# Performance work log

Hardware: AMD Instinct MI355X
Metric: run time of the kernel (lower is better)

Reference implementation:

```python
import jax, jax.numpy as jnp
import numpy as np

SHIFTS = (1, 2)          # _GLOBAL_SHIFTS, all < channels so none filtered
LN_EPS = 1e-5


def _layernorm(x, g, b):
    mu = jnp.mean(x, axis=-1, keepdims=True)
    var = jnp.var(x, axis=-1, keepdims=True)
    return (x - mu) * jax.lax.rsqrt(var + LN_EPS) * g + b


def setup_inputs() -> dict:
    key = jax.random.key(0)
    ks = jax.random.split(key, 4)
    B, H, W, D = 8, 96, 96, 256
    n_comp = 2 * len(SHIFTS)  # full mode: dot + wedge per shift
    x = jax.random.normal(ks[0], (B, H, W, D), dtype=jnp.float32)
    # glorot-uniform style scaling for the two dense kernels
    pk = jax.random.normal(ks[1], (n_comp * D, D), dtype=jnp.float32) * (1.0 / np.sqrt(n_comp * D))
    gk = jax.random.normal(ks[2], (2 * D, D), dtype=jnp.float32) * (1.0 / np.sqrt(2 * D))
    return {
        "x": x,
        "ln_gamma": jnp.ones((D,), jnp.float32),
        "ln_beta": jnp.zeros((D,), jnp.float32),
        "proj_kernel": pk,
        "proj_bias": jnp.zeros((D,), jnp.float32),
        "gate_kernel": gk,
        "gate_bias": jnp.zeros((D,), jnp.float32),
        "gamma": jnp.full((D,), 1e-5, jnp.float32),  # LayerScale init
    }


def reference(x, ln_gamma, ln_beta, proj_kernel, proj_bias,
              gate_kernel, gate_bias, gamma):
    # ---- pre-norm ----
    h_norm = _layernorm(x, ln_gamma, ln_beta)                 # [B,H,W,D]
    # ---- context stream (ctx_mode='diff'): deviation from spatial mean ----
    z_det = h_norm
    z_ctx = h_norm - jnp.mean(h_norm, axis=(1, 2), keepdims=True)
    # ---- sparse rolling Clifford product (cli_mode='full') ----
    feats = []
    for s in SHIFTS:
        ctx_s = jnp.roll(z_ctx, -s, axis=-1)   # Z_ctx[(c+s) % D]
        det_s = jnp.roll(z_det, -s, axis=-1)   # Z_det[(c+s) % D]
        dot = jax.nn.silu(z_det * ctx_s)                      # inner part
        wedge = z_det * ctx_s - z_ctx * det_s                 # bivector part
        feats.append(dot)
        feats.append(wedge)
    feats = jnp.concatenate(feats, axis=-1)                   # [B,H,W,4D]
    g_feat = feats @ proj_kernel + proj_bias                  # [B,H,W,D]
    # ---- gated geometric residual ----
    gate_in = jnp.concatenate([h_norm, g_feat], axis=-1)      # [B,H,W,2D]
    alpha = jax.nn.sigmoid(gate_in @ gate_kernel + gate_bias)
    h_mix = (jax.nn.silu(h_norm) + alpha * g_feat) * gamma    # LayerScale
    # drop_path_rate == 0.0 -> identity; caller-side residual add
    return x + h_mix
```

## Files before the change

### kernel.cpp

```cpp
#include <hip/hip_runtime.h>
#include <hip/hip_bf16.h>

typedef unsigned short u16;
typedef unsigned int   u32;
typedef __attribute__((ext_vector_type(2))) float f32x2;
typedef __attribute__((ext_vector_type(4))) float f32x4;
typedef __attribute__((ext_vector_type(4))) u32   u32x4;
typedef __attribute__((ext_vector_type(8))) short bf16x8;

#define HWPIX  9216
#define NPIX   73728
#define LN_EPS 1e-5f
#define MROW   64
#define ASTR   40

template<int N> struct IC { static constexpr int value = N; };

__device__ __forceinline__ u16 f2bf(float f){
  u32 u = __builtin_bit_cast(u32, f);
  u += 0x7fffu + ((u >> 16) & 1u);
  return (u16)(u >> 16);
}
__device__ __forceinline__ u32 pkbf(float lo, float hi){
  u32 d;
  asm("v_cvt_pk_bf16_f32 %0, %1, %2" : "=v"(d) : "v"(lo), "v"(hi));
  return d;
}
__device__ __forceinline__ float bfu2f(u16 h){ return __builtin_bit_cast(float, (u32)h << 16); }
__device__ __forceinline__ float fsigmoid(float v){ return __fdividef(1.f, 1.f + __expf(-v)); }
__device__ __forceinline__ float fsilu(float v){ return __fdividef(v, 1.f + __expf(-v)); }

__device__ __forceinline__ void gld16(const u16* g, u16* l){
  __builtin_amdgcn_global_load_lds((const __attribute__((address_space(1))) void*)g,
                                   (__attribute__((address_space(3))) void*)l,
                                   16, 0, 0);
}

__global__ __launch_bounds__(256) void wconv(const float* __restrict__ pk,
                                             const float* __restrict__ gk,
                                             u16* __restrict__ wsdot,
                                             u16* __restrict__ wsgate)
{
  int gid = blockIdx.x * 256 + threadIdx.x;
  int t = gid >> 10, S = gid & 1023;
  int q = (S >> 2) & 15, pp = S & 3, w8 = (S >> 6) & 7, rb = S >> 9;
  int n  = rb * 128 + w8 * 16 + q;
  int kq = pp ^ ((q >> 1) & 3);
  const float* W; int k0; u16* dst;
  if (t < 8)       { W = pk; k0 =       t      * 32 + kq * 8; dst = wsdot  + (size_t)t * 8192; }
  else if (t < 16) { W = pk; k0 = 512 + (t-8)  * 32 + kq * 8; dst = wsdot  + (size_t)t * 8192; }
  else             { W = gk; k0 =       (t-16) * 32 + kq * 8; dst = wsgate + (size_t)(t-16) * 8192; }
  u32 ow[4];
  #pragma unroll
  for (int e = 0; e < 4; ++e) {
    float f0 = W[(size_t)(k0 + 2*e)     * 256 + n];
    float f1 = W[(size_t)(k0 + 2*e + 1) * 256 + n];
    ow[e] = (u32)f2bf(f0) | ((u32)f2bf(f1) << 16);
  }
  *(u32x4*)(dst + (size_t)S * 8) = (u32x4){ow[0], ow[1], ow[2], ow[3]};
}

__global__ __launch_bounds__(256) void prep(const float* __restrict__ x,
                                            const float* __restrict__ g,
                                            const float* __restrict__ bt,
                                            float* __restrict__ mu_rs,
                                            float* __restrict__ partial)
{
  const int bh = blockIdx.x;
  const int tid = threadIdx.x;
  const int wv = tid >> 6, lane = tid & 63;
  const float* xrow = x + (size_t)bh * 96 * 256;
  __shared__ float red[4][256];

  f32x4 gv = *(const f32x4*)(g  + lane * 4);
  f32x4 bv = *(const f32x4*)(bt + lane * 4);
  f32x4 acc = {0.f, 0.f, 0.f, 0.f};

  for (int w = wv; w < 96; w += 4) {
    f32x4 v = *(const f32x4*)(xrow + w * 256 + lane * 4);
    float s  = v[0] + v[1] + v[2] + v[3];
    float s2 = v[0]*v[0] + v[1]*v[1] + v[2]*v[2] + v[3]*v[3];
    #pragma unroll
    for (int m = 1; m < 64; m <<= 1) { s += __shfl_xor(s, m); s2 += __shfl_xor(s2, m); }
    float mu  = s * (1.f / 256.f);
    float var = s2 * (1.f / 256.f) - mu * mu;
    float rs  = rsqrtf(var + LN_EPS);
    if (lane == 0) *(f32x2*)(mu_rs + (size_t)(bh * 96 + w) * 2) = f32x2{mu, rs};
    #pragma unroll
    for (int j = 0; j < 4; ++j) acc[j] += (v[j] - mu) * rs * gv[j] + bv[j];
  }
  *(f32x4*)(&red[wv][lane * 4]) = acc;
  __syncthreads();
  float s = red[0][tid] + red[1][tid] + red[2][tid] + red[3][tid];
  partial[(size_t)bh * 256 + tid] = s;
}

__global__ __launch_bounds__(256) void ln_mean(const float* __restrict__ partial,
                                               float* __restrict__ mean)
{
  int b = blockIdx.x, c = threadIdx.x;
  float s = 0.f;
  for (int h = 0; h < 96; ++h) s += partial[((size_t)b * 96 + h) * 256 + c];
  float m = s * (1.f / 9216.f);
  mean[b * 258 + c] = m;
  if (c < 2) mean[b * 258 + 256 + c] = m;
}

__global__ __launch_bounds__(256) void wfold(const float* __restrict__ pk,
                                             const float* __restrict__ meang,
                                             u16* __restrict__ wsW)
{
  __shared__ float msh[256];
  int gid = blockIdx.x * 256 + threadIdx.x;
  int chunk = gid >> 10;
  int b = chunk >> 3, j = chunk & 7;
  msh[threadIdx.x] = meang[b * 258 + threadIdx.x];
  __syncthreads();
  int S = gid & 1023;
  int q = (S >> 2) & 15, pp = S & 3, w8 = (S >> 6) & 7, rb = S >> 9;
  int n  = rb * 128 + w8 * 16 + q;
  int kq = pp ^ ((q >> 1) & 3);
  u32 ow[4];
  #pragma unroll
  for (int e = 0; e < 4; ++e) {
    float r[2];
    #pragma unroll
    for (int hh = 0; hh < 2; ++hh) {
      int c = j * 32 + kq * 8 + 2 * e + hh;
      int cm1 = (c + 255) & 255, cm2 = (c + 254) & 255;
      int cp1 = (c + 1) & 255,   cp2 = (c + 2) & 255;
      r[hh] = msh[cm1] * pk[(size_t)(256 + cm1) * 256 + n]
            - msh[cp1] * pk[(size_t)(256 + c)   * 256 + n]
            + msh[cm2] * pk[(size_t)(768 + cm2) * 256 + n]
            - msh[cp2] * pk[(size_t)(768 + c)   * 256 + n];
    }
    ow[e] = (u32)f2bf(r[0]) | ((u32)f2bf(r[1]) << 16);
  }
  *(u32x4*)(wsW + (size_t)chunk * 8192 + (size_t)S * 8) = (u32x4){ow[0], ow[1], ow[2], ow[3]};
}

__global__ __launch_bounds__(512, 2) void fused(
    const float* __restrict__ x,
    const float* __restrict__ lng, const float* __restrict__ lnb,
    const u16* __restrict__ wsdot, const u16* __restrict__ wsW,
    const u16* __restrict__ wsgate, const float* __restrict__ mu_rs,
    const float* __restrict__ pbias, const float* __restrict__ gbias,
    const float* __restrict__ gamma, const float* __restrict__ meang,
    float* __restrict__ out)
{
  __shared__ u16 afg[2][MROW * ASTR];
  __shared__ u16 Bl [3][8192];
  __shared__ float gshb[2][260];
  __shared__ float msh[258];
  __shared__ float mursh[128];

  const int tid  = threadIdx.x;
  const long pix0 = (long)blockIdx.x * MROW;
  const int bat  = (int)(pix0 / HWPIX);

  const int wave = tid >> 6, lane = tid & 63;
  const int wr = wave & 1, wc = wave >> 1;
  const int fr = lane & 15, kq = lane >> 4;
  const int bswz = (kq ^ ((fr >> 1) & 3)) * 8;
  const int brow = tid >> 3, o4 = (tid & 7) * 4;

  auto sgbase = [&](auto SEGC) -> const u16* {
    constexpr int sg = decltype(SEGC)::value;
    if constexpr      (sg == 0) return wsdot;
    else if constexpr (sg == 1) return wsdot + 8 * 8192;
    else if constexpr (sg == 2) return wsW + (size_t)bat * 65536;
    else if constexpr (sg == 3) return wsgate;
    else                        return wsgate + 8 * 8192;
  };
  auto stage = [&](auto UC, auto SL) {
    constexpr int u  = decltype(UC)::value;
    constexpr int sl = decltype(SL)::value;
    const u16* src = sgbase(IC<(u >> 3)>{}) + (size_t)(u & 7) * 8192 + tid * 8;
    u16* dst = &Bl[sl][wave * 512];
    gld16(src, dst);
    gld16(src + 4096, dst + 4096);
  };

  stage(IC<0>{}, IC<0>{});
  stage(IC<1>{}, IC<1>{});

  if (tid < 256)      { gshb[0][tid] = lng[tid]; gshb[1][tid] = lnb[tid]; }
  else if (tid < 260) { int c = tid - 256; gshb[0][256 + c] = lng[c]; gshb[1][256 + c] = lnb[c]; }
  if (tid < 258) msh[tid] = meang[bat * 258 + tid];
  if (tid < 128) mursh[tid] = mu_rs[pix0 * 2 + tid];

  f32x4 acc[2][4];
  #pragma unroll
  for (int i = 0; i < 2; ++i)
    #pragma unroll
    for (int j = 0; j < 4; ++j) acc[i][j] = (f32x4){0.f, 0.f, 0.f, 0.f};
  u32 gfp[2][4][2];
  float pbv[4];
  #pragma unroll
  for (int nt = 0; nt < 4; ++nt) pbv[nt] = pbias[wc * 64 + nt * 16 + fr];

  __syncthreads();

  const float* xrowp = x + (pix0 + brow) * 256;
  const float muv = mursh[brow * 2];
  const float rsv = mursh[brow * 2 + 1];

  auto featsB = [&](auto SC, int w, int buf) {
    constexpr int s = decltype(SC)::value;
    const int cc = w * 32 + o4;
    f32x4 xa = *(const f32x4*)(xrowp + cc);
    f32x4 xb = (cc == 252) ? *(const f32x4*)(xrowp) : *(const f32x4*)(xrowp + cc + 4);
    float h[8];
    #pragma unroll
    for (int j = 0; j < 4; ++j) h[j]     = (xa[j] - muv) * rsv * gshb[0][cc + j]     + gshb[1][cc + j];
    #pragma unroll
    for (int j = 0; j < 4; ++j) h[4 + j] = (xb[j] - muv) * rsv * gshb[0][cc + 4 + j] + gshb[1][cc + 4 + j];
    float r0 = fsilu(h[0] * (h[0 + s] - msh[cc + s]));
    float r1 = fsilu(h[1] * (h[1 + s] - msh[cc + 1 + s]));
    float r2 = fsilu(h[2] * (h[2 + s] - msh[cc + 2 + s]));
    float r3 = fsilu(h[3] * (h[3 + s] - msh[cc + 3 + s]));
    *(u32*)(&afg[buf][brow * ASTR + o4])     = pkbf(r0, r1);
    *(u32*)(&afg[buf][brow * ASTR + o4 + 2]) = pkbf(r2, r3);
  };
  auto hB = [&](int w, int buf) {
    const int cc = w * 32 + o4;
    f32x4 xa = *(const f32x4*)(xrowp + cc);
    float h0 = (xa[0] - muv) * rsv * gshb[0][cc]     + gshb[1][cc];
    float h1 = (xa[1] - muv) * rsv * gshb[0][cc + 1] + gshb[1][cc + 1];
    float h2 = (xa[2] - muv) * rsv * gshb[0][cc + 2] + gshb[1][cc + 2];
    float h3 = (xa[3] - muv) * rsv * gshb[0][cc + 3] + gshb[1][cc + 3];
    *(u32*)(&afg[buf][brow * ASTR + o4])     = pkbf(h0, h1);
    *(u32*)(&afg[buf][brow * ASTR + o4 + 2]) = pkbf(h2, h3);
  };
  auto gfcopy = [&](auto CGC, int buf) {
    constexpr int cg = decltype(CGC)::value;
    constexpr int par = cg & 1;
    if (wc == (cg >> 1)) {
      #pragma unroll
      for (int v = 0; v < 2; ++v) {
        #pragma unroll
        for (int ai = 0; ai < 2; ++ai)
          #pragma unroll
          for (int rp = 0; rp < 2; ++rp) {
            u32 pw = gfp[ai][par * 2 + v][rp];
            int row0 = wr * 32 + ai * 16 + kq * 4 + rp * 2;
            afg[buf][row0 * ASTR + v * 16 + fr]       = (u16)pw;
            afg[buf][(row0 + 1) * ASTR + v * 16 + fr] = (u16)(pw >> 16);
          }
      }
    }
  };

  auto domfma = [&](auto AB, auto SL) {
    constexpr int ab = decltype(AB)::value, sl = decltype(SL)::value;
    const u16* ar = &afg[ab][(wr * 32 + fr) * ASTR + kq * 8];
    bf16x8 av0 = *(const bf16x8*)(ar);
    bf16x8 av1 = *(const bf16x8*)(ar + 16 * ASTR);
    const u16* bp = &Bl[sl][wc * 2048 + fr * 32 + bswz];
    __builtin_amdgcn_s_setprio(1);
    #pragma unroll
    for (int nt = 0; nt < 4; ++nt) {
      bf16x8 bv = *(const bf16x8*)(bp + nt * 512);
      acc[0][nt] = __builtin_amdgcn_mfma_f32_16x16x32_bf16(av0, bv, acc[0][nt], 0, 0, 0);
      acc[1][nt] = __builtin_amdgcn_mfma_f32_16x16x32_bf16(av1, bv, acc[1][nt], 0, 0, 0);
    }
    __builtin_amdgcn_s_setprio(0);
  };

  featsB(IC<1>{}, 0, 0);
  asm volatile("s_waitcnt lgkmcnt(0)" ::: "memory");
  __builtin_amdgcn_s_barrier();

  auto stepfn = [&](auto TC) {
    constexpr int t = decltype(TC)::value;
    constexpr int u = t + 1;
    if constexpr (u < 8)       featsB(IC<1>{}, u & 7, u & 1);
    else if constexpr (u < 16) featsB(IC<2>{}, u & 7, u & 1);
    else if constexpr (u < 32) hB(u & 7, u & 1);
    else if constexpr (u < 40) gfcopy(IC<u - 32>{}, u & 1);
    domfma(IC<t & 1>{}, IC<t % 3>{});
    if constexpr (t == 23) {
      #pragma unroll
      for (int nt = 0; nt < 4; ++nt)
        #pragma unroll
        for (int ai = 0; ai < 2; ++ai) {
          f32x4 a = acc[ai][nt];
          gfp[ai][nt][0] = pkbf(a[0] + pbv[nt], a[1] + pbv[nt]);
          gfp[ai][nt][1] = pkbf(a[2] + pbv[nt], a[3] + pbv[nt]);
          acc[ai][nt] = (f32x4){0.f, 0.f, 0.f, 0.f};
        }
    }
    if constexpr (t + 2 < 40) stage(IC<t + 2>{}, IC<(t + 2) % 3>{});
    if constexpr (t < 37) asm volatile("s_waitcnt vmcnt(2) lgkmcnt(0)" ::: "memory");
    else                  asm volatile("s_waitcnt vmcnt(0) lgkmcnt(0)" ::: "memory");
    __builtin_amdgcn_s_barrier();
  };
  auto run8 = [&](auto B8) {
    constexpr int b8 = decltype(B8)::value;
    stepfn(IC<b8 + 0>{}); stepfn(IC<b8 + 1>{}); stepfn(IC<b8 + 2>{}); stepfn(IC<b8 + 3>{});
    stepfn(IC<b8 + 4>{}); stepfn(IC<b8 + 5>{}); stepfn(IC<b8 + 6>{}); stepfn(IC<b8 + 7>{});
  };
  run8(IC<0>{}); run8(IC<8>{}); run8(IC<16>{}); run8(IC<24>{}); run8(IC<32>{});

  float gbv[4], gmv[4];
  #pragma unroll
  for (int nt = 0; nt < 4; ++nt) {
    int col = wc * 64 + nt * 16 + fr;
    gbv[nt] = gbias[col]; gmv[nt] = gamma[col];
  }
  #pragma unroll
  for (int ai = 0; ai < 2; ++ai)
    #pragma unroll
    for (int rr = 0; rr < 4; ++rr) {
      const int row = wr * 32 + ai * 16 + kq * 4 + rr;
      const long pix = pix0 + row;
      const float mu2 = mursh[row * 2], rs2 = mursh[row * 2 + 1];
      #pragma unroll
      for (int nt = 0; nt < 4; ++nt) {
        int col = wc * 64 + nt * 16 + fr;
        float xv = x[pix * 256 + col];
        float hh = (xv - mu2) * rs2 * gshb[0][col] + gshb[1][col];
        u32 pw = gfp[ai][nt][rr >> 1];
        float gfv = bfu2f((u16)((rr & 1) ? (pw >> 16) : pw));
        float al = fsigmoid(acc[ai][nt][rr] + gbv[nt]);
        out[pix * 256 + col] = xv + (fsilu(hh) + al * gfv) * gmv[nt];
      }
    }
}

extern "C" void kernel_launch(void* const* d_in, const int* in_sizes, int n_in,
                              void* d_out, int out_size, void* d_ws, size_t ws_size,
                              hipStream_t stream) {
  const float* x     = (const float*)d_in[0];
  const float* lng   = (const float*)d_in[1];
  const float* lnb   = (const float*)d_in[2];
  const float* pk    = (const float*)d_in[3];
  const float* pbias = (const float*)d_in[4];
  const float* gk    = (const float*)d_in[5];
  const float* gbias = (const float*)d_in[6];
  const float* gamma = (const float*)d_in[7];
  float* out = (float*)d_out;

  char* ws = (char*)d_ws;
  u16*   wsdot   = (u16*)ws;
  u16*   wsgate  = (u16*)(ws + 262144);
  float* meang   = (float*)(ws + 524288);
  u16*   wsW     = (u16*)(ws + 532544);
  float* partial = (float*)(ws + 532544);
  float* mu_rs   = (float*)(ws + 1581120);

  wconv<<<128, 256, 0, stream>>>(pk, gk, wsdot, wsgate);
  prep<<<768, 256, 0, stream>>>(x, lng, lnb, mu_rs, partial);
  ln_mean<<<8, 256, 0, stream>>>(partial, meang);
  wfold<<<256, 256, 0, stream>>>(pk, meang, wsW);
  fused<<<NPIX / MROW, 512, 0, stream>>>(x, lng, lnb, wsdot, wsW, wsgate, mu_rs,
                                         pbias, gbias, gamma, meang, out);
}
```

Measured before the change: 151.3 us.

## Interleave gate-h GEMM with projection K-steps to share per-window x loads

Restructures the fused kernel's K-loop so that each 32-channel window computes h once and builds the dot(s=1), dot(s=2) and h A-tiles in consecutive steps. The h-part of the gate GEMM accumulates into a second accumulator set alongside the projection GEMM. This removes the repeated global x reads and LayerNorm recomputation across the three separate phases and cuts the step count from 40 to 32. In exchange it uses a fourth B staging buffer in LDS, doubles the accumulator registers, and reorders the weight layout so dot chunks for the two shifts interleave.

```diff
diff --git a/kernel.cpp b/kernel.cpp
--- a/kernel.cpp
+++ b/kernel.cpp
@@ -47,9 +47,8 @@
   int n  = rb * 128 + w8 * 16 + q;
   int kq = pp ^ ((q >> 1) & 3);
   const float* W; int k0; u16* dst;
-  if (t < 8)       { W = pk; k0 =       t      * 32 + kq * 8; dst = wsdot  + (size_t)t * 8192; }
-  else if (t < 16) { W = pk; k0 = 512 + (t-8)  * 32 + kq * 8; dst = wsdot  + (size_t)t * 8192; }
-  else             { W = gk; k0 =       (t-16) * 32 + kq * 8; dst = wsgate + (size_t)(t-16) * 8192; }
+  if (t < 16) { W = pk; k0 = (t & 1) * 512 + (t >> 1) * 32 + kq * 8; dst = wsdot + (size_t)t * 8192; }
+  else        { W = gk; k0 = (t - 16) * 32 + kq * 8;                 dst = wsgate + (size_t)(t - 16) * 8192; }
   u32 ow[4];
   #pragma unroll
   for (int e = 0; e < 4; ++e) {
@@ -149,7 +148,7 @@
     float* __restrict__ out)
 {
   __shared__ u16 afg[2][MROW * ASTR];
-  __shared__ u16 Bl [3][8192];
+  __shared__ u16 Bl [4][8192];
   __shared__ float gshb[2][260];
   __shared__ float msh[258];
   __shared__ float mursh[128];
@@ -164,36 +163,38 @@
   const int bswz = (kq ^ ((fr >> 1) & 3)) * 8;
   const int brow = tid >> 3, o4 = (tid & 7) * 4;
 
-  auto sgbase = [&](auto SEGC) -> const u16* {
-    constexpr int sg = decltype(SEGC)::value;
-    if constexpr      (sg == 0) return wsdot;
-    else if constexpr (sg == 1) return wsdot + 8 * 8192;
-    else if constexpr (sg == 2) return wsW + (size_t)bat * 65536;
-    else if constexpr (sg == 3) return wsgate;
-    else                        return wsgate + 8 * 8192;
-  };
-  auto stage = [&](auto UC, auto SL) {
-    constexpr int u  = decltype(UC)::value;
-    constexpr int sl = decltype(SL)::value;
-    const u16* src = sgbase(IC<(u >> 3)>{}) + (size_t)(u & 7) * 8192 + tid * 8;
+  auto stageQ = [&](auto QC) {
+    constexpr int q = decltype(QC)::value;
+    constexpr int sl = q & 3;
+    const u16* base;
+    if constexpr (q < 32) {
+      constexpr int w = q >> 2, r = q & 3;
+      if constexpr      (r == 0) base = wsdot  + (size_t)(2 * w)     * 8192;
+      else if constexpr (r == 1) base = wsdot  + (size_t)(2 * w + 1) * 8192;
+      else if constexpr (r == 2) base = wsW + (size_t)bat * 65536 + (size_t)w * 8192;
+      else                       base = wsgate + (size_t)w * 8192;
+    } else {
+      base = wsgate + (size_t)(q - 24) * 8192;
+    }
+    const u16* src = base + tid * 8;
     u16* dst = &Bl[sl][wave * 512];
     gld16(src, dst);
     gld16(src + 4096, dst + 4096);
   };
 
-  stage(IC<0>{}, IC<0>{});
-  stage(IC<1>{}, IC<1>{});
+  stageQ(IC<0>{});
+  stageQ(IC<1>{});
 
   if (tid < 256)      { gshb[0][tid] = lng[tid]; gshb[1][tid] = lnb[tid]; }
   else if (tid < 260) { int c = tid - 256; gshb[0][256 + c] = lng[c]; gshb[1][256 + c] = lnb[c]; }
   if (tid < 258) msh[tid] = meang[bat * 258 + tid];
   if (tid < 128) mursh[tid] = mu_rs[pix0 * 2 + tid];
 
-  f32x4 acc[2][4];
+  f32x4 accG[2][4], accA[2][4];
   #pragma unroll
   for (int i = 0; i < 2; ++i)
     #pragma unroll
-    for (int j = 0; j < 4; ++j) acc[i][j] = (f32x4){0.f, 0.f, 0.f, 0.f};
+    for (int j = 0; j < 4; ++j) { accG[i][j] = (f32x4){0,0,0,0}; accA[i][j] = (f32x4){0,0,0,0}; }
   u32 gfp[2][4][2];
   float pbv[4];
   #pragma unroll
@@ -205,30 +206,33 @@
   const float muv = mursh[brow * 2];
   const float rsv = mursh[brow * 2 + 1];
 
-  auto featsB = [&](auto SC, int w, int buf) {
+  float h0, h1, h2, h3, h4, h5;
+  auto computeH = [&](int w) {
+    const int cc = w * 32 + o4;
+    f32x4 xa = *(const f32x4*)(xrowp + cc);
+    f32x2 xb = (cc == 252) ? f32x2{xrowp[0], xrowp[1]}
+                           : *(const f32x2*)(xrowp + cc + 4);
+    h0 = (xa[0] - muv) * rsv * gshb[0][cc]     + gshb[1][cc];
+    h1 = (xa[1] - muv) * rsv * gshb[0][cc + 1] + gshb[1][cc + 1];
+    h2 = (xa[2] - muv) * rsv * gshb[0][cc + 2] + gshb[1][cc + 2];
+    h3 = (xa[3] - muv) * rsv * gshb[0][cc + 3] + gshb[1][cc + 3];
+    h4 = (xb[0] - muv) * rsv * gshb[0][cc + 4] + gshb[1][cc + 4];
+    h5 = (xb[1] - muv) * rsv * gshb[0][cc + 5] + gshb[1][cc + 5];
+  };
+  auto buildDot = [&](auto SC, int w, int buf) {
     constexpr int s = decltype(SC)::value;
     const int cc = w * 32 + o4;
-    f32x4 xa = *(const f32x4*)(xrowp + cc);
-    f32x4 xb = (cc == 252) ? *(const f32x4*)(xrowp) : *(const f32x4*)(xrowp + cc + 4);
-    float h[8];
-    #pragma unroll
-    for (int j = 0; j < 4; ++j) h[j]     = (xa[j] - muv) * rsv * gshb[0][cc + j]     + gshb[1][cc + j];
-    #pragma unroll
-    for (int j = 0; j < 4; ++j) h[4 + j] = (xb[j] - muv) * rsv * gshb[0][cc + 4 + j] + gshb[1][cc + 4 + j];
-    float r0 = fsilu(h[0] * (h[0 + s] - msh[cc + s]));
-    float r1 = fsilu(h[1] * (h[1 + s] - msh[cc + 1 + s]));
-    float r2 = fsilu(h[2] * (h[2 + s] - msh[cc + 2 + s]));
-    float r3 = fsilu(h[3] * (h[3 + s] - msh[cc + 3 + s]));
+    float a0, a1, a2, a3;
+    if constexpr (s == 1) { a0 = h1; a1 = h2; a2 = h3; a3 = h4; }
+    else                  { a0 = h2; a1 = h3; a2 = h4; a3 = h5; }
+    float r0 = fsilu(h0 * (a0 - msh[cc + s]));
+    float r1 = fsilu(h1 * (a1 - msh[cc + 1 + s]));
+    float r2 = fsilu(h2 * (a2 - msh[cc + 2 + s]));
+    float r3 = fsilu(h3 * (a3 - msh[cc + 3 + s]));
     *(u32*)(&afg[buf][brow * ASTR + o4])     = pkbf(r0, r1);
     *(u32*)(&afg[buf][brow * ASTR + o4 + 2]) = pkbf(r2, r3);
   };
-  auto hB = [&](int w, int buf) {
-    const int cc = w * 32 + o4;
-    f32x4 xa = *(const f32x4*)(xrowp + cc);
-    float h0 = (xa[0] - muv) * rsv * gshb[0][cc]     + gshb[1][cc];
-    float h1 = (xa[1] - muv) * rsv * gshb[0][cc + 1] + gshb[1][cc + 1];
-    float h2 = (xa[2] - muv) * rsv * gshb[0][cc + 2] + gshb[1][cc + 2];
-    float h3 = (xa[3] - muv) * rsv * gshb[0][cc + 3] + gshb[1][cc + 3];
+  auto buildH = [&](int buf) {
     *(u32*)(&afg[buf][brow * ASTR + o4])     = pkbf(h0, h1);
     *(u32*)(&afg[buf][brow * ASTR + o4 + 2]) = pkbf(h2, h3);
   };
@@ -251,48 +255,75 @@
     }
   };
 
-  auto domfma = [&](auto AB, auto SL) {
-    constexpr int ab = decltype(AB)::value, sl = decltype(SL)::value;
-    const u16* ar = &afg[ab][(wr * 32 + fr) * ASTR + kq * 8];
+  auto mfma_into = [&](f32x4 (&ac)[2][4], int abuf, const u16* bp) {
+    const u16* ar = &afg[abuf][(wr * 32 + fr) * ASTR + kq * 8];
     bf16x8 av0 = *(const bf16x8*)(ar);
     bf16x8 av1 = *(const bf16x8*)(ar + 16 * ASTR);
-    const u16* bp = &Bl[sl][wc * 2048 + fr * 32 + bswz];
     __builtin_amdgcn_s_setprio(1);
     #pragma unroll
     for (int nt = 0; nt < 4; ++nt) {
       bf16x8 bv = *(const bf16x8*)(bp + nt * 512);
-      acc[0][nt] = __builtin_amdgcn_mfma_f32_16x16x32_bf16(av0, bv, acc[0][nt], 0, 0, 0);
-      acc[1][nt] = __builtin_amdgcn_mfma_f32_16x16x32_bf16(av1, bv, acc[1][nt], 0, 0, 0);
+      ac[0][nt] = __builtin_amdgcn_mfma_f32_16x16x32_bf16(av0, bv, ac[0][nt], 0, 0, 0);
+      ac[1][nt] = __builtin_amdgcn_mfma_f32_16x16x32_bf16(av1, bv, ac[1][nt], 0, 0, 0);
     }
     __builtin_amdgcn_s_setprio(0);
   };
 
-  featsB(IC<1>{}, 0, 0);
+  computeH(0);
+  buildDot(IC<1>{}, 0, 0);
   asm volatile("s_waitcnt lgkmcnt(0)" ::: "memory");
   __builtin_amdgcn_s_barrier();
 
   auto stepfn = [&](auto TC) {
     constexpr int t = decltype(TC)::value;
     constexpr int u = t + 1;
-    if constexpr (u < 8)       featsB(IC<1>{}, u & 7, u & 1);
-    else if constexpr (u < 16) featsB(IC<2>{}, u & 7, u & 1);
-    else if constexpr (u < 32) hB(u & 7, u & 1);
-    else if constexpr (u < 40) gfcopy(IC<u - 32>{}, u & 1);
-    domfma(IC<t & 1>{}, IC<t % 3>{});
+    if constexpr (u < 24) {
+      constexpr int r3 = u % 3, w = u / 3;
+      if constexpr (r3 == 0)      { computeH(w); buildDot(IC<1>{}, w, u & 1); }
+      else if constexpr (r3 == 1) buildDot(IC<2>{}, u / 3, u & 1);
+      else                        buildH(u & 1);
+    } else if constexpr (u >= 25 && u < 32) {
+      gfcopy(IC<u - 24>{}, u & 1);
+    }
+    if constexpr (t < 24) {
+      constexpr int g = t / 3, r3 = t % 3;
+      if constexpr (r3 < 2) {
+        constexpr int q = 4 * g + r3;
+        mfma_into(accG, t & 1, &Bl[q & 3][wc * 2048 + fr * 32 + bswz]);
+      } else {
+        constexpr int q = 4 * g + 2;
+        mfma_into(accG, t & 1, &Bl[q & 3][wc * 2048 + fr * 32 + bswz]);
+        mfma_into(accA, t & 1, &Bl[(q + 1) & 3][wc * 2048 + fr * 32 + bswz]);
+      }
+    } else {
+      constexpr int q = t + 8;
+      mfma_into(accA, t & 1, &Bl[q & 3][wc * 2048 + fr * 32 + bswz]);
+    }
     if constexpr (t == 23) {
       #pragma unroll
       for (int nt = 0; nt < 4; ++nt)
         #pragma unroll
         for (int ai = 0; ai < 2; ++ai) {
-          f32x4 a = acc[ai][nt];
+          f32x4 a = accG[ai][nt];
           gfp[ai][nt][0] = pkbf(a[0] + pbv[nt], a[1] + pbv[nt]);
           gfp[ai][nt][1] = pkbf(a[2] + pbv[nt], a[3] + pbv[nt]);
-          acc[ai][nt] = (f32x4){0.f, 0.f, 0.f, 0.f};
         }
-    }
-    if constexpr (t + 2 < 40) stage(IC<t + 2>{}, IC<(t + 2) % 3>{});
-    if constexpr (t < 37) asm volatile("s_waitcnt vmcnt(2) lgkmcnt(0)" ::: "memory");
-    else                  asm volatile("s_waitcnt vmcnt(0) lgkmcnt(0)" ::: "memory");
+      gfcopy(IC<0>{}, 0);
+    }
+    if constexpr (t + 2 < 32) {
+      constexpr int s2 = t + 2;
+      constexpr int nq = (s2 < 24) ? ((s2 % 3 == 2) ? 2 : 1) : 1;
+      constexpr int q0 = (s2 < 24) ? (4 * (s2 / 3) + s2 % 3) : (s2 + 8);
+      stageQ(IC<q0>{});
+      if constexpr (nq == 2) {
+        stageQ(IC<q0 + 1>{});
+        asm volatile("s_waitcnt vmcnt(4) lgkmcnt(0)" ::: "memory");
+      } else {
+        asm volatile("s_waitcnt vmcnt(2) lgkmcnt(0)" ::: "memory");
+      }
+    } else {
+      asm volatile("s_waitcnt vmcnt(0) lgkmcnt(0)" ::: "memory");
+    }
     __builtin_amdgcn_s_barrier();
   };
   auto run8 = [&](auto B8) {
@@ -300,7 +331,7 @@
     stepfn(IC<b8 + 0>{}); stepfn(IC<b8 + 1>{}); stepfn(IC<b8 + 2>{}); stepfn(IC<b8 + 3>{});
     stepfn(IC<b8 + 4>{}); stepfn(IC<b8 + 5>{}); stepfn(IC<b8 + 6>{}); stepfn(IC<b8 + 7>{});
   };
-  run8(IC<0>{}); run8(IC<8>{}); run8(IC<16>{}); run8(IC<24>{}); run8(IC<32>{});
+  run8(IC<0>{}); run8(IC<8>{}); run8(IC<16>{}); run8(IC<24>{});
 
   float gbv[4], gmv[4];
   #pragma unroll
@@ -322,7 +353,7 @@
         float hh = (xv - mu2) * rs2 * gshb[0][col] + gshb[1][col];
         u32 pw = gfp[ai][nt][rr >> 1];
         float gfv = bfu2f((u16)((rr & 1) ? (pw >> 16) : pw));
-        float al = fsigmoid(acc[ai][nt][rr] + gbv[nt]);
+        float al = fsigmoid(accA[ai][nt][rr] + gbv[nt]);
         out[pix * 256 + col] = xv + (fsilu(hh) + al * gfv) * gmv[nt];
       }
     }
```

Result: slower. 164.0 us (+8.4%).
